# Kernel optimization log

Hardware: AMD Instinct MI355X
Metric: run time of the kernel (lower is better)

## Reference

```python
import jax, jax.numpy as jnp
import numpy as np

B = 65536      # batch
E = 4          # experts per node
F = 32         # per-node input features
H = 256        # hidden width
NODES = 4
D_MID = 128    # intermediate node output dim
D_OUT = 8      # final head dim


def _lin_w(k, fan_in, fan_out):
    b = 1.0 / np.sqrt(fan_in)
    return jax.random.uniform(k, (E, fan_in, fan_out), jnp.float32, -b, b)


def setup_inputs() -> dict:
    key = jax.random.key(0)
    ks = jax.random.split(key, 8)
    feats = jax.random.normal(ks[0], (B, NODES * F), dtype=jnp.float32)
    # routing one-hot blocks embedded in the input vector (as the module expects)
    ohs = [jax.nn.one_hot(jax.random.randint(ks[1 + j], (B,), 0, E), E, dtype=jnp.float32)
           for j in range(NODES)]
    input_val = jnp.concatenate([feats] + ohs, axis=1)  # [B, 144]
    p = {"input_val": input_val}
    kc = iter(jax.random.split(ks[5], 32))
    # node 0: no pre-interface; post: F->H relu, H->D_MID relu
    p["W0_0"] = _lin_w(next(kc), F, H); p["b0_0"] = jnp.full((E, H), 0.1, jnp.float32)
    p["W0_1"] = _lin_w(next(kc), H, D_MID); p["b0_1"] = jnp.full((E, D_MID), 0.1, jnp.float32)
    # nodes 1,2: pre F->H relu; post (D_MID+H)->H relu, H->D_MID relu
    for j in (1, 2):
        p[f"W{j}_pre"] = _lin_w(next(kc), F, H); p[f"b{j}_pre"] = jnp.full((E, H), 0.1, jnp.float32)
        p[f"W{j}_0"] = _lin_w(next(kc), D_MID + H, H); p[f"b{j}_0"] = jnp.full((E, H), 0.1, jnp.float32)
        p[f"W{j}_1"] = _lin_w(next(kc), H, D_MID); p[f"b{j}_1"] = jnp.full((E, D_MID), 0.1, jnp.float32)
    # node 3 (output): pre F->H relu; post (D_MID+H)->H relu, H->D_OUT identity
    p["W3_pre"] = _lin_w(next(kc), F, H); p["b3_pre"] = jnp.full((E, H), 0.1, jnp.float32)
    p["W3_0"] = _lin_w(next(kc), D_MID + H, H); p["b3_0"] = jnp.full((E, H), 0.1, jnp.float32)
    p["W3_1"] = jax.random.uniform(next(kc), (E, H, D_OUT), jnp.float32, -0.003, 0.003)
    p["b3_1"] = jax.random.uniform(next(kc), (E, D_OUT), jnp.float32, -0.003, 0.003)
    return p


def reference(input_val, W0_0, b0_0, W0_1, b0_1,
              W1_pre, b1_pre, W1_0, b1_0, W1_1, b1_1,
              W2_pre, b2_pre, W2_0, b2_0, W2_1, b2_1,
              W3_pre, b3_pre, W3_0, b3_0, W3_1, b3_1):
    relu = jax.nn.relu
    xs = [input_val[:, j * F:(j + 1) * F] for j in range(NODES)]          # per-node features
    ohs = [input_val[:, NODES * F + j * E: NODES * F + (j + 1) * E] for j in range(NODES)]

    def combine(oh, outs):  # oh [B,E] exact one-hot; outs [E,B,D] -> exact per-row expert pick
        return jnp.einsum('be,ebo->bo', oh, outs)

    # node 0 (no previous-level input)
    def n0(W0, b0, W1, b1):
        h = relu(xs[0] @ W0 + b0)
        return relu(h @ W1 + b1)
    x = combine(ohs[0], jax.vmap(n0)(W0_0, b0_0, W0_1, b0_1))  # [B, D_MID]

    def node(xj, xprev, relu_last):
        def f(Wp, bp, W0, b0, W1, b1):
            h = relu(xj @ Wp + bp)                      # pre-interface
            h = jnp.concatenate([xprev, h], axis=-1)    # interface: cat(prev, pre)
            h = relu(h @ W0 + b0)
            o = h @ W1 + b1
            return relu(o) if relu_last else o
        return f

    x = combine(ohs[1], jax.vmap(node(xs[1], x, True))(W1_pre, b1_pre, W1_0, b1_0, W1_1, b1_1))
    x = combine(ohs[2], jax.vmap(node(xs[2], x, True))(W2_pre, b2_pre, W2_0, b2_0, W2_1, b2_1))
    x = combine(ohs[3], jax.vmap(node(xs[3], x, False))(W3_pre, b3_pre, W3_0, b3_0, W3_1, b3_1))
    return x  # [B, D_OUT]
```

## Files before the change

kernel.cpp:

```cpp
#include <hip/hip_runtime.h>
#include <hip/hip_bf16.h>
#include <stdint.h>

typedef unsigned int u32;
typedef unsigned short u16;
typedef unsigned char u8;
typedef __bf16 bf16x8 __attribute__((ext_vector_type(8)));
typedef float f32x4 __attribute__((ext_vector_type(4)));

#define NB 65536
#define NBLK 1280
#define PERM_TOT (NBLK * 64)
#define INVR 0xFFFFFFFFu
#define BLK_DEAD 0xFFFFu

#define O_ROWS 0
#define O_XJ   256
#define O_P    (O_XJ + 4096)
#define O_H    (O_P + 16384)
#define O_RED  O_P
#define SM_BYTES (O_H + 32768)

__device__ __host__ constexpr int TS(int m) {
  constexpr int t[12] = {0, 64, 320, 384, 1152, 1408, 1472, 2240, 2496, 2560, 3328, 3360};
  return t[m];
}

__device__ __forceinline__ u16 f2bf(float f) {
  u32 u = __builtin_bit_cast(u32, f);
  u32 r = (u + 0x7FFFu + ((u >> 16) & 1u)) >> 16;
  return (u16)r;
}
__device__ __forceinline__ float relu_f(float x) { return x > 0.f ? x : 0.f; }
__device__ __forceinline__ f32x4 mfma16(bf16x8 a, bf16x8 b, f32x4 c) {
  return __builtin_amdgcn_mfma_f32_16x16x32_bf16(a, b, c, 0, 0, 0);
}

__device__ __forceinline__ void mkpair(f32x4 acc, float bias, bool dorelu, int l16,
                                       u32& w0, u32& w1) {
  float v0 = acc[0] + bias, v1 = acc[1] + bias, v2 = acc[2] + bias, v3 = acc[3] + bias;
  if (dorelu) { v0 = relu_f(v0); v1 = relu_f(v1); v2 = relu_f(v2); v3 = relu_f(v3); }
  u32 a = (u32)f2bf(v0) | ((u32)f2bf(v1) << 16);
  u32 b = (u32)f2bf(v2) | ((u32)f2bf(v3) << 16);
  u32 ax = (u32)__shfl_xor((int)a, 1);
  u32 bx = (u32)__shfl_xor((int)b, 1);
  if ((l16 & 1) == 0) { w0 = (a & 0xffffu) | (ax << 16); w1 = (a >> 16) | (ax & 0xffff0000u); }
  else                { w0 = (bx & 0xffffu) | (b << 16); w1 = (bx >> 16) | (b & 0xffff0000u); }
}

__device__ __forceinline__ void frag_store_pair(char* base, int KT, int m0, int col,
                                                u32 w0, u32 w1) {
  char* d = base + (((m0 >> 4) * KT + (col >> 5)) << 10) +
            (((m0 & 15) + (((col & 31) >> 3) << 4)) << 4) + (col & 7) * 2;
  *(u32*)d = w0; *(u32*)(d + 16) = w1;
}


struct PrepArgs {
  const float* src[11];
  int K[11], Nsrc[11];
  int tileStart[12];
};

__device__ __forceinline__ void prep_tile_dev(__bf16* __restrict__ pk, const PrepArgs& pa,
                                              int gt, int lane) {
  const int quad = lane >> 4, l16 = lane & 15;
  int m = 0;
  while (gt >= pa.tileStart[m + 1]) m++;
  const int loc = gt - pa.tileStart[m];
  const int K = pa.K[m], Ns = pa.Nsrc[m];
  const int Np = Ns < 16 ? 16 : Ns;
  const int KT = K >> 5, NT = Np >> 4;
  const int e = loc / (KT * NT), rem = loc % (KT * NT);
  const int nt = rem / KT, kt = rem % KT;
  const int k = kt * 32 + quad * 8, n = nt * 16 + l16;
  u32 hw[4];
  if (n < Ns) {
    const float* s = pa.src[m] + ((size_t)e * K + k) * Ns + n;
    u16 h[8];
#pragma unroll
    for (int j = 0; j < 8; j++) h[j] = f2bf(s[(size_t)j * Ns]);
    hw[0] = (u32)h[0] | ((u32)h[1] << 16);
    hw[1] = (u32)h[2] | ((u32)h[3] << 16);
    hw[2] = (u32)h[4] | ((u32)h[5] << 16);
    hw[3] = (u32)h[6] | ((u32)h[7] << 16);
  } else {
    hw[0] = hw[1] = hw[2] = hw[3] = 0u;
  }
  uint4 w; w.x = hw[0]; w.y = hw[1]; w.z = hw[2]; w.w = hw[3];
  *(uint4*)((char*)pk + (size_t)gt * 1024 + lane * 16) = w;
}


__global__ __launch_bounds__(256) void k_front(const float* __restrict__ inp,
                                               u8* __restrict__ bkt,
                                               u32* __restrict__ cnt2,
                                               u32* __restrict__ rank,
                                               __bf16* __restrict__ pk, PrepArgs pa) {
  __shared__ u32 h[256];
  const int tid = threadIdx.x;
  if (blockIdx.x == 0) rank[tid] = 0u;
  h[tid] = 0u;
  __syncthreads();
  const int r = blockIdx.x * 256 + tid;
  const float4* oh = (const float4*)(inp + (size_t)r * 144 + 128);
  u32 b = 0;
#pragma unroll
  for (int j = 0; j < 4; j++) {
    float4 v = oh[j];
    u32 e = v.y > 0.5f ? 1u : (v.z > 0.5f ? 2u : (v.w > 0.5f ? 3u : 0u));
    b |= e << (2 * j);
  }
  bkt[r] = (u8)b;
  atomicAdd(&h[b], 1u);
  __syncthreads();
  cnt2[blockIdx.x * 256 + tid] = h[tid];
  for (int g4 = blockIdx.x; g4 < TS(11) / 4; g4 += 256)
    prep_tile_dev(pk, pa, g4 * 4 + (tid >> 6), tid & 63);
}


__global__ __launch_bounds__(256) void k_place(const u8* __restrict__ bkt,
                                               const u32* __restrict__ cnt2,
                                               u32* __restrict__ rank,
                                               u16* __restrict__ blk2b,
                                               u32* __restrict__ perm) {
  __shared__ u32 s[256], base[256];
  const int tid = threadIdx.x;
  u32 c = 0;
#pragma unroll 8
  for (int j = 0; j < 256; j++) c += cnt2[j * 256 + tid];
  const u32 pad = (c + 63u) & ~63u;
  s[tid] = pad;
  __syncthreads();
  for (int d = 1; d < 256; d <<= 1) {
    u32 v = (tid >= d) ? s[tid - d] : 0u;
    __syncthreads();
    s[tid] += v;
    __syncthreads();
  }
  const u32 off = s[tid] - pad;
  const u32 total = s[255];
  __syncthreads();
  if (blockIdx.x == 0) {
    for (u32 i = off + c; i < off + pad; i++) perm[i] = INVR;
    for (u32 blk = off >> 6; blk < (off + pad) >> 6; blk++) blk2b[blk] = (u16)tid;
    for (u32 blk = (total >> 6) + tid; blk < NBLK; blk += 256) blk2b[blk] = BLK_DEAD;
  }
  s[tid] = 0u;
  __syncthreads();
  const int r = blockIdx.x * 256 + tid;
  const u32 b = bkt[r];
  const u32 lrk = atomicAdd(&s[b], 1u);
  __syncthreads();
  base[tid] = off + (s[tid] ? atomicAdd(&rank[tid], s[tid]) : 0u);
  __syncthreads();
  perm[base[b] + lrk] = (u32)r;
}


__device__ __forceinline__ void xj_load(const float* inp, u32 myrow, int tid, int node,
                                        float4& v0, float4& v1) {
  v0 = make_float4(0.f, 0.f, 0.f, 0.f); v1 = v0;
  if (myrow != INVR) {
    const int c8 = (tid & 3) << 3;
    const float4* p = (const float4*)(inp + (size_t)myrow * 144 + node * 32 + c8);
    v0 = p[0]; v1 = p[1];
  }
}

__device__ __forceinline__ void xj_store(char* sm, int tid, float4 v0, float4 v1) {
  const int r = tid >> 2;
  uint4 w;
  w.x = (u32)f2bf(v0.x) | ((u32)f2bf(v0.y) << 16);
  w.y = (u32)f2bf(v0.z) | ((u32)f2bf(v0.w) << 16);
  w.z = (u32)f2bf(v1.x) | ((u32)f2bf(v1.y) << 16);
  w.w = (u32)f2bf(v1.z) | ((u32)f2bf(v1.w) << 16);
  *(uint4*)(sm + O_XJ + ((r >> 4) << 10) + ((((tid & 3) << 4) + (r & 15)) << 4)) = w;
}

__device__ __forceinline__ void pre_gemm(char* sm, u32 e, int wave, int lane,
                                         const __bf16* Wp, const float* bp) {
  const int l16 = lane & 15;
  const int wn0 = wave * 64;
  const int rsel = ((lane >> 4) << 2) + ((l16 & 1) ? 2 : 0);
  const int colp = l16 & ~1;
  float bias[4];
#pragma unroll
  for (int nt = 0; nt < 4; nt++) bias[nt] = bp[(size_t)e * 256 + wn0 + nt * 16 + l16];
  f32x4 acc[4][4];
#pragma unroll
  for (int i = 0; i < 4; i++)
#pragma unroll
    for (int j = 0; j < 4; j++) acc[i][j] = (f32x4){0.f, 0.f, 0.f, 0.f};
  bf16x8 a[4], b[4];
#pragma unroll
  for (int nt = 0; nt < 4; nt++)
    b[nt] = *(const bf16x8*)(Wp + (size_t)(e * 16 + (wn0 >> 4) + nt) * 512 + lane * 8);
#pragma unroll
  for (int mt = 0; mt < 4; mt++)
    a[mt] = *(const bf16x8*)(sm + O_XJ + (mt << 10) + lane * 16);
#pragma unroll
  for (int mt = 0; mt < 4; mt++)
#pragma unroll
    for (int nt = 0; nt < 4; nt++) acc[mt][nt] = mfma16(a[mt], b[nt], acc[mt][nt]);
#pragma unroll
  for (int nt = 0; nt < 4; nt++) {
    const int n = wn0 + nt * 16;
#pragma unroll
    for (int mt = 0; mt < 4; mt++) {
      u32 w0, w1;
      mkpair(acc[mt][nt], bias[nt], true, l16, w0, w1);
      frag_store_pair(sm + O_H, 8, mt * 16 + rsel, n + colp, w0, w1);
    }
  }
}

__device__ __forceinline__ void main_gemm(char* sm, u32 e, int wave, int lane,
                                          const __bf16* Wm, const float* bm) {
  const int l16 = lane & 15;
  const int wn0 = wave * 64;
  const int rsel = ((lane >> 4) << 2) + ((l16 & 1) ? 2 : 0);
  const int colp = l16 & ~1;
  float bias[4];
#pragma unroll
  for (int nt = 0; nt < 4; nt++) bias[nt] = bm[(size_t)e * 256 + wn0 + nt * 16 + l16];
  f32x4 acc[4][4];
#pragma unroll
  for (int i = 0; i < 4; i++)
#pragma unroll
    for (int j = 0; j < 4; j++) acc[i][j] = (f32x4){0.f, 0.f, 0.f, 0.f};
  const __bf16* bB = Wm + (size_t)(e * 16 + (wn0 >> 4)) * 12 * 512 + lane * 8;
  bf16x8 bb[2][4];
#pragma unroll
  for (int nt = 0; nt < 4; nt++) {
    bb[0][nt] = *(const bf16x8*)(bB + (size_t)(nt * 12 + 0) * 512);
    bb[1][nt] = *(const bf16x8*)(bB + (size_t)(nt * 12 + 1) * 512);
  }
#pragma unroll
  for (int kt = 0; kt < 12; kt++) {
    bf16x8 a[4];
#pragma unroll
    for (int mt = 0; mt < 4; mt++) {
      a[mt] = (kt < 4)
          ? *(const bf16x8*)(sm + O_P + ((mt * 4 + kt) << 10) + lane * 16)
          : *(const bf16x8*)(sm + O_H + ((mt * 8 + (kt - 4)) << 10) + lane * 16);
    }
#pragma unroll
    for (int mt = 0; mt < 4; mt++)
#pragma unroll
      for (int nt = 0; nt < 4; nt++) acc[mt][nt] = mfma16(a[mt], bb[kt & 1][nt], acc[mt][nt]);
    if (kt < 10) {
#pragma unroll
      for (int nt = 0; nt < 4; nt++)
        bb[kt & 1][nt] = *(const bf16x8*)(bB + (size_t)(nt * 12 + kt + 2) * 512);
    }
  }
  __syncthreads();
#pragma unroll
  for (int nt = 0; nt < 4; nt++) {
    const int n = wn0 + nt * 16;
#pragma unroll
    for (int mt = 0; mt < 4; mt++) {
      u32 w0, w1;
      mkpair(acc[mt][nt], bias[nt], true, l16, w0, w1);
      frag_store_pair(sm + O_H, 8, mt * 16 + rsel, n + colp, w0, w1);
    }
  }
  __syncthreads();
}

__device__ __forceinline__ void out_gemm(char* sm, u32 e, int wave, int lane,
                                         const __bf16* Wo, const float* bo) {
  const int l16 = lane & 15;
  const int on0 = wave * 32;
  const int rsel = ((lane >> 4) << 2) + ((l16 & 1) ? 2 : 0);
  const int colp = l16 & ~1;
  float bias[2];
#pragma unroll
  for (int nt = 0; nt < 2; nt++) bias[nt] = bo[(size_t)e * 128 + on0 + nt * 16 + l16];
  f32x4 acc[4][2];
#pragma unroll
  for (int i = 0; i < 4; i++) { acc[i][0] = (f32x4){0.f,0.f,0.f,0.f}; acc[i][1] = acc[i][0]; }
  const __bf16* bB = Wo + (size_t)(e * 8 + (on0 >> 4)) * 8 * 512 + lane * 8;
  bf16x8 bb[2][2];
#pragma unroll
  for (int nt = 0; nt < 2; nt++) {
    bb[0][nt] = *(const bf16x8*)(bB + (size_t)(nt * 8 + 0) * 512);
    bb[1][nt] = *(const bf16x8*)(bB + (size_t)(nt * 8 + 1) * 512);
  }
#pragma unroll
  for (int kt = 0; kt < 8; kt++) {
    bf16x8 a[4];
#pragma unroll
    for (int mt = 0; mt < 4; mt++)
      a[mt] = *(const bf16x8*)(sm + O_H + ((mt * 8 + kt) << 10) + lane * 16);
#pragma unroll
    for (int mt = 0; mt < 4; mt++)
#pragma unroll
      for (int nt = 0; nt < 2; nt++) acc[mt][nt] = mfma16(a[mt], bb[kt & 1][nt], acc[mt][nt]);
    if (kt < 6) {
#pragma unroll
      for (int nt = 0; nt < 2; nt++)
        bb[kt & 1][nt] = *(const bf16x8*)(bB + (size_t)(nt * 8 + kt + 2) * 512);
    }
  }
#pragma unroll
  for (int nt = 0; nt < 2; nt++) {
    const int n = on0 + nt * 16;
#pragma unroll
    for (int mt = 0; mt < 4; mt++) {
      u32 w0, w1;
      mkpair(acc[mt][nt], bias[nt], true, l16, w0, w1);
      frag_store_pair(sm + O_P, 4, mt * 16 + rsel, n + colp, w0, w1);
    }
  }
}

__global__ __launch_bounds__(256, 3) void fused_k(
    const float* __restrict__ inp, const u32* __restrict__ perm,
    const u16* __restrict__ blk2b, const __bf16* __restrict__ pk,
    const float* __restrict__ b0_0, const float* __restrict__ b0_1,
    const float* __restrict__ b1_p, const float* __restrict__ b1_0,
    const float* __restrict__ b1_1, const float* __restrict__ b2_p,
    const float* __restrict__ b2_0, const float* __restrict__ b2_1,
    const float* __restrict__ b3_p, const float* __restrict__ b3_0,
    const float* __restrict__ b3_1, float* __restrict__ dout) {
  const u32 b = blk2b[blockIdx.x];
  if (b == BLK_DEAD) return;
  __shared__ __align__(16) char sm[SM_BYTES];
  u32* rows = (u32*)sm;
  const int tid = threadIdx.x;
  const int wave = tid >> 6, lane = tid & 63, quad = lane >> 4, l16 = lane & 15;
  if (tid < 64) rows[tid] = perm[blockIdx.x * 64 + tid];
  const u32 e0 = b & 3u, e1 = (b >> 2) & 3u, e2 = (b >> 4) & 3u, e3 = (b >> 6) & 3u;
  __syncthreads();
  const u32 myrow = rows[tid >> 2];

  float4 v0, v1;
  xj_load(inp, myrow, tid, 0, v0, v1);
  xj_store(sm, tid, v0, v1);
  __syncthreads();
  pre_gemm(sm, e0, wave, lane, pk + (size_t)TS(0) * 512, b0_0);
  __syncthreads();
  xj_load(inp, myrow, tid, 1, v0, v1);
  out_gemm(sm, e0, wave, lane, pk + (size_t)TS(1) * 512, b0_1);
  xj_store(sm, tid, v0, v1);
  __syncthreads();
  pre_gemm(sm, e1, wave, lane, pk + (size_t)TS(2) * 512, b1_p);
  __syncthreads();
  main_gemm(sm, e1, wave, lane, pk + (size_t)TS(3) * 512, b1_0);
  xj_load(inp, myrow, tid, 2, v0, v1);
  out_gemm(sm, e1, wave, lane, pk + (size_t)TS(4) * 512, b1_1);
  xj_store(sm, tid, v0, v1);
  __syncthreads();
  pre_gemm(sm, e2, wave, lane, pk + (size_t)TS(5) * 512, b2_p);
  __syncthreads();
  main_gemm(sm, e2, wave, lane, pk + (size_t)TS(6) * 512, b2_0);
  xj_load(inp, myrow, tid, 3, v0, v1);
  out_gemm(sm, e2, wave, lane, pk + (size_t)TS(7) * 512, b2_1);
  xj_store(sm, tid, v0, v1);
  __syncthreads();
  pre_gemm(sm, e3, wave, lane, pk + (size_t)TS(8) * 512, b3_p);
  __syncthreads();
  main_gemm(sm, e3, wave, lane, pk + (size_t)TS(9) * 512, b3_0);

  {
    const __bf16* Wo3 = pk + (size_t)TS(10) * 512;
    f32x4 acc3[4];
#pragma unroll
    for (int i = 0; i < 4; i++) acc3[i] = (f32x4){0.f, 0.f, 0.f, 0.f};
#pragma unroll
    for (int kk = 0; kk < 2; kk++) {
      const int kt = wave * 2 + kk;
      bf16x8 b3 = *(const bf16x8*)(Wo3 + (size_t)(e3 * 8 + kt) * 512 + lane * 8);
      bf16x8 a[4];
#pragma unroll
      for (int mt = 0; mt < 4; mt++)
        a[mt] = *(const bf16x8*)(sm + O_H + ((mt * 8 + kt) << 10) + lane * 16);
#pragma unroll
      for (int mt = 0; mt < 4; mt++) acc3[mt] = mfma16(a[mt], b3, acc3[mt]);
    }
#pragma unroll
    for (int mt = 0; mt < 4; mt++)
#pragma unroll
      for (int r = 0; r < 4; r++)
        *(float*)(sm + O_RED +
                  (((size_t)wave * 64 + mt * 16 + quad * 4 + r) * 16 + l16) * 4) = acc3[mt][r];
    __syncthreads();
    const int m = tid >> 2, c = (tid & 3) * 2;
    float s0 = 0.f, s1 = 0.f;
#pragma unroll
    for (int w = 0; w < 4; w++) {
      s0 += *(float*)(sm + O_RED + (((size_t)w * 64 + m) * 16 + c) * 4);
      s1 += *(float*)(sm + O_RED + (((size_t)w * 64 + m) * 16 + c + 1) * 4);
    }
    if (myrow != INVR) {
      float2 o;
      o.x = s0 + b3_1[(size_t)e3 * 8 + c];
      o.y = s1 + b3_1[(size_t)e3 * 8 + c + 1];
      *(float2*)(dout + (size_t)myrow * 8 + c) = o;
    }
  }
}


extern "C" void kernel_launch(void* const* d_in, const int* in_sizes, int n_in,
                              void* d_out, int out_size, void* d_ws, size_t ws_size,
                              hipStream_t stream) {
  (void)in_sizes; (void)n_in; (void)out_size; (void)ws_size;
  const float* inp = (const float*)d_in[0];
  char* ws = (char*)d_ws;

  const size_t oBKT = 0;
  const size_t oRANK = oBKT + NB;
  const size_t oB2B = oRANK + 1024;
  const size_t oCNT2 = (oB2B + NBLK * 2 + 255) & ~(size_t)255;
  const size_t oPERM = oCNT2 + 256 * 256 * 4;
  const size_t oPK = (oPERM + (size_t)PERM_TOT * 4 + 255) & ~(size_t)255;

  u8* bkt = (u8*)(ws + oBKT);
  u32* rank = (u32*)(ws + oRANK);
  u16* blk2b = (u16*)(ws + oB2B);
  u32* cnt2 = (u32*)(ws + oCNT2);
  u32* perm = (u32*)(ws + oPERM);
  __bf16* pk = (__bf16*)(ws + oPK);

  PrepArgs pa;
  const int widx[11] = {1, 3, 5, 7, 9, 11, 13, 15, 17, 19, 21};
  const int Ks[11] = {32, 256, 32, 384, 256, 32, 384, 256, 32, 384, 256};
  const int Ns[11] = {256, 128, 256, 256, 128, 256, 256, 128, 256, 256, 8};
  for (int m = 0; m < 11; m++) {
    pa.src[m] = (const float*)d_in[widx[m]];
    pa.K[m] = Ks[m]; pa.Nsrc[m] = Ns[m]; pa.tileStart[m] = TS(m);
  }
  pa.tileStart[11] = TS(11);

  hipLaunchKernelGGL(k_front, dim3(NB / 256), dim3(256), 0, stream,
                     inp, bkt, cnt2, rank, pk, pa);
  hipLaunchKernelGGL(k_place, dim3(NB / 256), dim3(256), 0, stream,
                     bkt, cnt2, rank, blk2b, perm);
  fused_k<<<NBLK, 256, 0, stream>>>(
      inp, perm, blk2b, pk,
      (const float*)d_in[2], (const float*)d_in[4],
      (const float*)d_in[6], (const float*)d_in[8], (const float*)d_in[10],
      (const float*)d_in[12], (const float*)d_in[14], (const float*)d_in[16],
      (const float*)d_in[18], (const float*)d_in[20], (const float*)d_in[22],
      (float*)d_out);
}
```

Before: 224.6 us.

## Use 512-thread blocks with eight waves splitting GEMM output columns

Doubles the fused kernel's block size to 512 threads so eight waves each compute half as many output columns in the pre, main and output GEMMs. Input staging and the final reduction stay on the first 256 threads or four waves. The aim is more wave-level parallelism and latency hiding per block with fewer accumulator registers per wave. The cost is that each wave now loads the same A fragments from LDS for half the MFMA work, and more threads take part in every barrier.

```diff
diff --git a/kernel.cpp b/kernel.cpp
--- a/kernel.cpp
+++ b/kernel.cpp
@@ -162,7 +162,7 @@
 __device__ __forceinline__ void xj_load(const float* inp, u32 myrow, int tid, int node,
                                         float4& v0, float4& v1) {
   v0 = make_float4(0.f, 0.f, 0.f, 0.f); v1 = v0;
-  if (myrow != INVR) {
+  if (tid < 256 && myrow != INVR) {
     const int c8 = (tid & 3) << 3;
     const float4* p = (const float4*)(inp + (size_t)myrow * 144 + node * 32 + c8);
     v0 = p[0]; v1 = p[1];
@@ -170,6 +170,7 @@
 }
 
 __device__ __forceinline__ void xj_store(char* sm, int tid, float4 v0, float4 v1) {
+  if (tid >= 256) return;
   const int r = tid >> 2;
   uint4 w;
   w.x = (u32)f2bf(v0.x) | ((u32)f2bf(v0.y) << 16);
@@ -182,20 +183,18 @@
 __device__ __forceinline__ void pre_gemm(char* sm, u32 e, int wave, int lane,
                                          const __bf16* Wp, const float* bp) {
   const int l16 = lane & 15;
-  const int wn0 = wave * 64;
+  const int wn0 = wave * 32;
   const int rsel = ((lane >> 4) << 2) + ((l16 & 1) ? 2 : 0);
   const int colp = l16 & ~1;
-  float bias[4];
-#pragma unroll
-  for (int nt = 0; nt < 4; nt++) bias[nt] = bp[(size_t)e * 256 + wn0 + nt * 16 + l16];
-  f32x4 acc[4][4];
-#pragma unroll
-  for (int i = 0; i < 4; i++)
-#pragma unroll
-    for (int j = 0; j < 4; j++) acc[i][j] = (f32x4){0.f, 0.f, 0.f, 0.f};
-  bf16x8 a[4], b[4];
-#pragma unroll
-  for (int nt = 0; nt < 4; nt++)
+  float bias[2];
+#pragma unroll
+  for (int nt = 0; nt < 2; nt++) bias[nt] = bp[(size_t)e * 256 + wn0 + nt * 16 + l16];
+  f32x4 acc[4][2];
+#pragma unroll
+  for (int i = 0; i < 4; i++) { acc[i][0] = (f32x4){0.f,0.f,0.f,0.f}; acc[i][1] = acc[i][0]; }
+  bf16x8 a[4], b[2];
+#pragma unroll
+  for (int nt = 0; nt < 2; nt++)
     b[nt] = *(const bf16x8*)(Wp + (size_t)(e * 16 + (wn0 >> 4) + nt) * 512 + lane * 8);
 #pragma unroll
   for (int mt = 0; mt < 4; mt++)
@@ -203,9 +202,9 @@
 #pragma unroll
   for (int mt = 0; mt < 4; mt++)
 #pragma unroll
-    for (int nt = 0; nt < 4; nt++) acc[mt][nt] = mfma16(a[mt], b[nt], acc[mt][nt]);
-#pragma unroll
-  for (int nt = 0; nt < 4; nt++) {
+    for (int nt = 0; nt < 2; nt++) acc[mt][nt] = mfma16(a[mt], b[nt], acc[mt][nt]);
+#pragma unroll
+  for (int nt = 0; nt < 2; nt++) {
     const int n = wn0 + nt * 16;
 #pragma unroll
     for (int mt = 0; mt < 4; mt++) {
@@ -219,21 +218,19 @@
 __device__ __forceinline__ void main_gemm(char* sm, u32 e, int wave, int lane,
                                           const __bf16* Wm, const float* bm) {
   const int l16 = lane & 15;
-  const int wn0 = wave * 64;
+  const int wn0 = wave * 32;
   const int rsel = ((lane >> 4) << 2) + ((l16 & 1) ? 2 : 0);
   const int colp = l16 & ~1;
-  float bias[4];
-#pragma unroll
-  for (int nt = 0; nt < 4; nt++) bias[nt] = bm[(size_t)e * 256 + wn0 + nt * 16 + l16];
-  f32x4 acc[4][4];
-#pragma unroll
-  for (int i = 0; i < 4; i++)
-#pragma unroll
-    for (int j = 0; j < 4; j++) acc[i][j] = (f32x4){0.f, 0.f, 0.f, 0.f};
+  float bias[2];
+#pragma unroll
+  for (int nt = 0; nt < 2; nt++) bias[nt] = bm[(size_t)e * 256 + wn0 + nt * 16 + l16];
+  f32x4 acc[4][2];
+#pragma unroll
+  for (int i = 0; i < 4; i++) { acc[i][0] = (f32x4){0.f,0.f,0.f,0.f}; acc[i][1] = acc[i][0]; }
   const __bf16* bB = Wm + (size_t)(e * 16 + (wn0 >> 4)) * 12 * 512 + lane * 8;
-  bf16x8 bb[2][4];
-#pragma unroll
-  for (int nt = 0; nt < 4; nt++) {
+  bf16x8 bb[2][2];
+#pragma unroll
+  for (int nt = 0; nt < 2; nt++) {
     bb[0][nt] = *(const bf16x8*)(bB + (size_t)(nt * 12 + 0) * 512);
     bb[1][nt] = *(const bf16x8*)(bB + (size_t)(nt * 12 + 1) * 512);
   }
@@ -249,16 +246,16 @@
 #pragma unroll
     for (int mt = 0; mt < 4; mt++)
 #pragma unroll
-      for (int nt = 0; nt < 4; nt++) acc[mt][nt] = mfma16(a[mt], bb[kt & 1][nt], acc[mt][nt]);
+      for (int nt = 0; nt < 2; nt++) acc[mt][nt] = mfma16(a[mt], bb[kt & 1][nt], acc[mt][nt]);
     if (kt < 10) {
 #pragma unroll
-      for (int nt = 0; nt < 4; nt++)
+      for (int nt = 0; nt < 2; nt++)
         bb[kt & 1][nt] = *(const bf16x8*)(bB + (size_t)(nt * 12 + kt + 2) * 512);
     }
   }
   __syncthreads();
 #pragma unroll
-  for (int nt = 0; nt < 4; nt++) {
+  for (int nt = 0; nt < 2; nt++) {
     const int n = wn0 + nt * 16;
 #pragma unroll
     for (int mt = 0; mt < 4; mt++) {
@@ -273,22 +270,17 @@
 __device__ __forceinline__ void out_gemm(char* sm, u32 e, int wave, int lane,
                                          const __bf16* Wo, const float* bo) {
   const int l16 = lane & 15;
-  const int on0 = wave * 32;
+  const int on0 = wave * 16;
   const int rsel = ((lane >> 4) << 2) + ((l16 & 1) ? 2 : 0);
   const int colp = l16 & ~1;
-  float bias[2];
-#pragma unroll
-  for (int nt = 0; nt < 2; nt++) bias[nt] = bo[(size_t)e * 128 + on0 + nt * 16 + l16];
-  f32x4 acc[4][2];
-#pragma unroll
-  for (int i = 0; i < 4; i++) { acc[i][0] = (f32x4){0.f,0.f,0.f,0.f}; acc[i][1] = acc[i][0]; }
+  const float bias0 = bo[(size_t)e * 128 + on0 + l16];
+  f32x4 acc[4];
+#pragma unroll
+  for (int i = 0; i < 4; i++) acc[i] = (f32x4){0.f, 0.f, 0.f, 0.f};
   const __bf16* bB = Wo + (size_t)(e * 8 + (on0 >> 4)) * 8 * 512 + lane * 8;
-  bf16x8 bb[2][2];
-#pragma unroll
-  for (int nt = 0; nt < 2; nt++) {
-    bb[0][nt] = *(const bf16x8*)(bB + (size_t)(nt * 8 + 0) * 512);
-    bb[1][nt] = *(const bf16x8*)(bB + (size_t)(nt * 8 + 1) * 512);
-  }
+  bf16x8 bb[2];
+  bb[0] = *(const bf16x8*)(bB);
+  bb[1] = *(const bf16x8*)(bB + 512);
 #pragma unroll
   for (int kt = 0; kt < 8; kt++) {
     bf16x8 a[4];
@@ -296,28 +288,18 @@
     for (int mt = 0; mt < 4; mt++)
       a[mt] = *(const bf16x8*)(sm + O_H + ((mt * 8 + kt) << 10) + lane * 16);
 #pragma unroll
-    for (int mt = 0; mt < 4; mt++)
-#pragma unroll
-      for (int nt = 0; nt < 2; nt++) acc[mt][nt] = mfma16(a[mt], bb[kt & 1][nt], acc[mt][nt]);
-    if (kt < 6) {
-#pragma unroll
-      for (int nt = 0; nt < 2; nt++)
-        bb[kt & 1][nt] = *(const bf16x8*)(bB + (size_t)(nt * 8 + kt + 2) * 512);
-    }
-  }
-#pragma unroll
-  for (int nt = 0; nt < 2; nt++) {
-    const int n = on0 + nt * 16;
-#pragma unroll
-    for (int mt = 0; mt < 4; mt++) {
-      u32 w0, w1;
-      mkpair(acc[mt][nt], bias[nt], true, l16, w0, w1);
-      frag_store_pair(sm + O_P, 4, mt * 16 + rsel, n + colp, w0, w1);
-    }
-  }
-}
-
-__global__ __launch_bounds__(256, 3) void fused_k(
+    for (int mt = 0; mt < 4; mt++) acc[mt] = mfma16(a[mt], bb[kt & 1], acc[mt]);
+    if (kt < 6) bb[kt & 1] = *(const bf16x8*)(bB + (size_t)(kt + 2) * 512);
+  }
+#pragma unroll
+  for (int mt = 0; mt < 4; mt++) {
+    u32 w0, w1;
+    mkpair(acc[mt], bias0, true, l16, w0, w1);
+    frag_store_pair(sm + O_P, 4, mt * 16 + rsel, on0 + colp, w0, w1);
+  }
+}
+
+__global__ __launch_bounds__(512, 6) void fused_k(
     const float* __restrict__ inp, const u32* __restrict__ perm,
     const u16* __restrict__ blk2b, const __bf16* __restrict__ pk,
     const float* __restrict__ b0_0, const float* __restrict__ b0_1,
@@ -335,7 +317,7 @@
   if (tid < 64) rows[tid] = perm[blockIdx.x * 64 + tid];
   const u32 e0 = b & 3u, e1 = (b >> 2) & 3u, e2 = (b >> 4) & 3u, e3 = (b >> 6) & 3u;
   __syncthreads();
-  const u32 myrow = rows[tid >> 2];
+  const u32 myrow = rows[(tid & 255) >> 2];
 
   float4 v0, v1;
   xj_load(inp, myrow, tid, 0, v0, v1);
@@ -367,39 +349,43 @@
 
   {
     const __bf16* Wo3 = pk + (size_t)TS(10) * 512;
-    f32x4 acc3[4];
-#pragma unroll
-    for (int i = 0; i < 4; i++) acc3[i] = (f32x4){0.f, 0.f, 0.f, 0.f};
-#pragma unroll
-    for (int kk = 0; kk < 2; kk++) {
-      const int kt = wave * 2 + kk;
-      bf16x8 b3 = *(const bf16x8*)(Wo3 + (size_t)(e3 * 8 + kt) * 512 + lane * 8);
-      bf16x8 a[4];
+    if (wave < 4) {
+      f32x4 acc3[4];
+#pragma unroll
+      for (int i = 0; i < 4; i++) acc3[i] = (f32x4){0.f, 0.f, 0.f, 0.f};
+#pragma unroll
+      for (int kk = 0; kk < 2; kk++) {
+        const int kt = wave * 2 + kk;
+        bf16x8 b3 = *(const bf16x8*)(Wo3 + (size_t)(e3 * 8 + kt) * 512 + lane * 8);
+        bf16x8 a[4];
+#pragma unroll
+        for (int mt = 0; mt < 4; mt++)
+          a[mt] = *(const bf16x8*)(sm + O_H + ((mt * 8 + kt) << 10) + lane * 16);
+#pragma unroll
+        for (int mt = 0; mt < 4; mt++) acc3[mt] = mfma16(a[mt], b3, acc3[mt]);
+      }
 #pragma unroll
       for (int mt = 0; mt < 4; mt++)
-        a[mt] = *(const bf16x8*)(sm + O_H + ((mt * 8 + kt) << 10) + lane * 16);
-#pragma unroll
-      for (int mt = 0; mt < 4; mt++) acc3[mt] = mfma16(a[mt], b3, acc3[mt]);
-    }
-#pragma unroll
-    for (int mt = 0; mt < 4; mt++)
-#pragma unroll
-      for (int r = 0; r < 4; r++)
-        *(float*)(sm + O_RED +
-                  (((size_t)wave * 64 + mt * 16 + quad * 4 + r) * 16 + l16) * 4) = acc3[mt][r];
+#pragma unroll
+        for (int r = 0; r < 4; r++)
+          *(float*)(sm + O_RED +
+                    (((size_t)wave * 64 + mt * 16 + quad * 4 + r) * 16 + l16) * 4) = acc3[mt][r];
+    }
     __syncthreads();
-    const int m = tid >> 2, c = (tid & 3) * 2;
-    float s0 = 0.f, s1 = 0.f;
-#pragma unroll
-    for (int w = 0; w < 4; w++) {
-      s0 += *(float*)(sm + O_RED + (((size_t)w * 64 + m) * 16 + c) * 4);
-      s1 += *(float*)(sm + O_RED + (((size_t)w * 64 + m) * 16 + c + 1) * 4);
-    }
-    if (myrow != INVR) {
-      float2 o;
-      o.x = s0 + b3_1[(size_t)e3 * 8 + c];
-      o.y = s1 + b3_1[(size_t)e3 * 8 + c + 1];
-      *(float2*)(dout + (size_t)myrow * 8 + c) = o;
+    if (tid < 256) {
+      const int m = tid >> 2, c = (tid & 3) * 2;
+      float s0 = 0.f, s1 = 0.f;
+#pragma unroll
+      for (int w = 0; w < 4; w++) {
+        s0 += *(float*)(sm + O_RED + (((size_t)w * 64 + m) * 16 + c) * 4);
+        s1 += *(float*)(sm + O_RED + (((size_t)w * 64 + m) * 16 + c + 1) * 4);
+      }
+      if (myrow != INVR) {
+        float2 o;
+        o.x = s0 + b3_1[(size_t)e3 * 8 + c];
+        o.y = s1 + b3_1[(size_t)e3 * 8 + c + 1];
+        *(float2*)(dout + (size_t)myrow * 8 + c) = o;
+      }
     }
   }
 }
@@ -440,7 +426,7 @@
                      inp, bkt, cnt2, rank, pk, pa);
   hipLaunchKernelGGL(k_place, dim3(NB / 256), dim3(256), 0, stream,
                      bkt, cnt2, rank, blk2b, perm);
-  fused_k<<<NBLK, 256, 0, stream>>>(
+  fused_k<<<NBLK, 512, 0, stream>>>(
       inp, perm, blk2b, pk,
       (const float*)d_in[2], (const float*)d_in[4],
       (const float*)d_in[6], (const float*)d_in[8], (const float*)d_in[10],
```

Measured after the change: 221.5 us. No clear change (-1.3%).

## Halve per-block row tile to 32 rows, raise occupancy, use packed bf16 convert

Applied to the files above, without the earlier changes.

Shrinks each fused block from 64 to 32 routed rows. This doubles the block count, halves shared memory and accumulator registers, and raises the launch-bounds occupancy hint from 3 to 6. Bucket padding becomes 32 rows, which reduces wasted padded rows across the 256 expert-combination buckets. The software-pipelined weight prefetch is dropped in favour of per-iteration loads, and float-to-bf16 conversion uses the v_cvt_pk_bf16_f32 instruction. Trade-off: weights are reloaded per 32 rows, so weight traffic per row doubles, and half the threads sit idle during input staging.

```diff
diff --git a/kernel.cpp b/kernel.cpp
--- a/kernel.cpp
+++ b/kernel.cpp
@@ -9,17 +9,16 @@
 typedef float f32x4 __attribute__((ext_vector_type(4)));
 
 #define NB 65536
-#define NBLK 1280
-#define PERM_TOT (NBLK * 64)
+#define NBLK 2560
+#define PERM_TOT (NBLK * 32)
 #define INVR 0xFFFFFFFFu
 #define BLK_DEAD 0xFFFFu
 
-#define O_ROWS 0
 #define O_XJ   256
-#define O_P    (O_XJ + 4096)
-#define O_H    (O_P + 16384)
+#define O_P    (O_XJ + 2048)
+#define O_H    (O_P + 8192)
 #define O_RED  O_P
-#define SM_BYTES (O_H + 32768)
+#define SM_BYTES (O_H + 16384)
 
 __device__ __host__ constexpr int TS(int m) {
   constexpr int t[12] = {0, 64, 320, 384, 1152, 1408, 1472, 2240, 2496, 2560, 3328, 3360};
@@ -31,17 +30,22 @@
   u32 r = (u + 0x7FFFu + ((u >> 16) & 1u)) >> 16;
   return (u16)r;
 }
+__device__ __forceinline__ u32 cvtpk(float lo, float hi) {
+  u32 r;
+  asm("v_cvt_pk_bf16_f32 %0, %1, %2" : "=v"(r) : "v"(lo), "v"(hi));
+  return r;
+}
 __device__ __forceinline__ float relu_f(float x) { return x > 0.f ? x : 0.f; }
 __device__ __forceinline__ f32x4 mfma16(bf16x8 a, bf16x8 b, f32x4 c) {
   return __builtin_amdgcn_mfma_f32_16x16x32_bf16(a, b, c, 0, 0, 0);
 }
 
-__device__ __forceinline__ void mkpair(f32x4 acc, float bias, bool dorelu, int l16,
+__device__ __forceinline__ void mkpair(f32x4 acc, float bias, int l16,
                                        u32& w0, u32& w1) {
-  float v0 = acc[0] + bias, v1 = acc[1] + bias, v2 = acc[2] + bias, v3 = acc[3] + bias;
-  if (dorelu) { v0 = relu_f(v0); v1 = relu_f(v1); v2 = relu_f(v2); v3 = relu_f(v3); }
-  u32 a = (u32)f2bf(v0) | ((u32)f2bf(v1) << 16);
-  u32 b = (u32)f2bf(v2) | ((u32)f2bf(v3) << 16);
+  float v0 = relu_f(acc[0] + bias), v1 = relu_f(acc[1] + bias);
+  float v2 = relu_f(acc[2] + bias), v3 = relu_f(acc[3] + bias);
+  u32 a = cvtpk(v0, v1);
+  u32 b = cvtpk(v2, v3);
   u32 ax = (u32)__shfl_xor((int)a, 1);
   u32 bx = (u32)__shfl_xor((int)b, 1);
   if ((l16 & 1) == 0) { w0 = (a & 0xffffu) | (ax << 16); w1 = (a >> 16) | (ax & 0xffff0000u); }
@@ -130,7 +134,7 @@
   u32 c = 0;
 #pragma unroll 8
   for (int j = 0; j < 256; j++) c += cnt2[j * 256 + tid];
-  const u32 pad = (c + 63u) & ~63u;
+  const u32 pad = (c + 31u) & ~31u;
   s[tid] = pad;
   __syncthreads();
   for (int d = 1; d < 256; d <<= 1) {
@@ -144,8 +148,8 @@
   __syncthreads();
   if (blockIdx.x == 0) {
     for (u32 i = off + c; i < off + pad; i++) perm[i] = INVR;
-    for (u32 blk = off >> 6; blk < (off + pad) >> 6; blk++) blk2b[blk] = (u16)tid;
-    for (u32 blk = (total >> 6) + tid; blk < NBLK; blk += 256) blk2b[blk] = BLK_DEAD;
+    for (u32 blk = off >> 5; blk < (off + pad) >> 5; blk++) blk2b[blk] = (u16)tid;
+    for (u32 blk = (total >> 5) + tid; blk < NBLK; blk += 256) blk2b[blk] = BLK_DEAD;
   }
   s[tid] = 0u;
   __syncthreads();
@@ -162,7 +166,7 @@
 __device__ __forceinline__ void xj_load(const float* inp, u32 myrow, int tid, int node,
                                         float4& v0, float4& v1) {
   v0 = make_float4(0.f, 0.f, 0.f, 0.f); v1 = v0;
-  if (myrow != INVR) {
+  if (tid < 128 && myrow != INVR) {
     const int c8 = (tid & 3) << 3;
     const float4* p = (const float4*)(inp + (size_t)myrow * 144 + node * 32 + c8);
     v0 = p[0]; v1 = p[1];
@@ -170,12 +174,13 @@
 }
 
 __device__ __forceinline__ void xj_store(char* sm, int tid, float4 v0, float4 v1) {
+  if (tid >= 128) return;
   const int r = tid >> 2;
   uint4 w;
-  w.x = (u32)f2bf(v0.x) | ((u32)f2bf(v0.y) << 16);
-  w.y = (u32)f2bf(v0.z) | ((u32)f2bf(v0.w) << 16);
-  w.z = (u32)f2bf(v1.x) | ((u32)f2bf(v1.y) << 16);
-  w.w = (u32)f2bf(v1.z) | ((u32)f2bf(v1.w) << 16);
+  w.x = cvtpk(v0.x, v0.y);
+  w.y = cvtpk(v0.z, v0.w);
+  w.z = cvtpk(v1.x, v1.y);
+  w.w = cvtpk(v1.z, v1.w);
   *(uint4*)(sm + O_XJ + ((r >> 4) << 10) + ((((tid & 3) << 4) + (r & 15)) << 4)) = w;
 }
 
@@ -188,29 +193,29 @@
   float bias[4];
 #pragma unroll
   for (int nt = 0; nt < 4; nt++) bias[nt] = bp[(size_t)e * 256 + wn0 + nt * 16 + l16];
-  f32x4 acc[4][4];
-#pragma unroll
-  for (int i = 0; i < 4; i++)
+  f32x4 acc[2][4];
+#pragma unroll
+  for (int i = 0; i < 2; i++)
 #pragma unroll
     for (int j = 0; j < 4; j++) acc[i][j] = (f32x4){0.f, 0.f, 0.f, 0.f};
-  bf16x8 a[4], b[4];
+  bf16x8 a[2], b[4];
 #pragma unroll
   for (int nt = 0; nt < 4; nt++)
-    b[nt] = *(const bf16x8*)(Wp + (size_t)(e * 16 + (wn0 >> 4) + nt) * 512 + lane * 8);
-#pragma unroll
-  for (int mt = 0; mt < 4; mt++)
+    b[nt] = *(const bf16x8*)(Wp + (size_t)(e * 16 + wave * 4 + nt) * 512 + lane * 8);
+#pragma unroll
+  for (int mt = 0; mt < 2; mt++)
     a[mt] = *(const bf16x8*)(sm + O_XJ + (mt << 10) + lane * 16);
 #pragma unroll
-  for (int mt = 0; mt < 4; mt++)
+  for (int mt = 0; mt < 2; mt++)
 #pragma unroll
     for (int nt = 0; nt < 4; nt++) acc[mt][nt] = mfma16(a[mt], b[nt], acc[mt][nt]);
 #pragma unroll
   for (int nt = 0; nt < 4; nt++) {
     const int n = wn0 + nt * 16;
 #pragma unroll
-    for (int mt = 0; mt < 4; mt++) {
+    for (int mt = 0; mt < 2; mt++) {
       u32 w0, w1;
-      mkpair(acc[mt][nt], bias[nt], true, l16, w0, w1);
+      mkpair(acc[mt][nt], bias[nt], l16, w0, w1);
       frag_store_pair(sm + O_H, 8, mt * 16 + rsel, n + colp, w0, w1);
     }
   }
@@ -225,45 +230,37 @@
   float bias[4];
 #pragma unroll
   for (int nt = 0; nt < 4; nt++) bias[nt] = bm[(size_t)e * 256 + wn0 + nt * 16 + l16];
-  f32x4 acc[4][4];
-#pragma unroll
-  for (int i = 0; i < 4; i++)
+  f32x4 acc[2][4];
+#pragma unroll
+  for (int i = 0; i < 2; i++)
 #pragma unroll
     for (int j = 0; j < 4; j++) acc[i][j] = (f32x4){0.f, 0.f, 0.f, 0.f};
-  const __bf16* bB = Wm + (size_t)(e * 16 + (wn0 >> 4)) * 12 * 512 + lane * 8;
-  bf16x8 bb[2][4];
-#pragma unroll
-  for (int nt = 0; nt < 4; nt++) {
-    bb[0][nt] = *(const bf16x8*)(bB + (size_t)(nt * 12 + 0) * 512);
-    bb[1][nt] = *(const bf16x8*)(bB + (size_t)(nt * 12 + 1) * 512);
-  }
+  const __bf16* bB = Wm + (size_t)(e * 16 + wave * 4) * 12 * 512 + lane * 8;
 #pragma unroll
   for (int kt = 0; kt < 12; kt++) {
-    bf16x8 a[4];
-#pragma unroll
-    for (int mt = 0; mt < 4; mt++) {
+    bf16x8 a[2], bb[4];
+#pragma unroll
+    for (int mt = 0; mt < 2; mt++) {
       a[mt] = (kt < 4)
           ? *(const bf16x8*)(sm + O_P + ((mt * 4 + kt) << 10) + lane * 16)
           : *(const bf16x8*)(sm + O_H + ((mt * 8 + (kt - 4)) << 10) + lane * 16);
     }
 #pragma unroll
-    for (int mt = 0; mt < 4; mt++)
-#pragma unroll
-      for (int nt = 0; nt < 4; nt++) acc[mt][nt] = mfma16(a[mt], bb[kt & 1][nt], acc[mt][nt]);
-    if (kt < 10) {
-#pragma unroll
-      for (int nt = 0; nt < 4; nt++)
-        bb[kt & 1][nt] = *(const bf16x8*)(bB + (size_t)(nt * 12 + kt + 2) * 512);
-    }
+    for (int nt = 0; nt < 4; nt++)
+      bb[nt] = *(const bf16x8*)(bB + (size_t)(nt * 12 + kt) * 512);
+#pragma unroll
+    for (int mt = 0; mt < 2; mt++)
+#pragma unroll
+      for (int nt = 0; nt < 4; nt++) acc[mt][nt] = mfma16(a[mt], bb[nt], acc[mt][nt]);
   }
   __syncthreads();
 #pragma unroll
   for (int nt = 0; nt < 4; nt++) {
     const int n = wn0 + nt * 16;
 #pragma unroll
-    for (int mt = 0; mt < 4; mt++) {
+    for (int mt = 0; mt < 2; mt++) {
       u32 w0, w1;
-      mkpair(acc[mt][nt], bias[nt], true, l16, w0, w1);
+      mkpair(acc[mt][nt], bias[nt], l16, w0, w1);
       frag_store_pair(sm + O_H, 8, mt * 16 + rsel, n + colp, w0, w1);
     }
   }
@@ -279,45 +276,37 @@
   float bias[2];
 #pragma unroll
   for (int nt = 0; nt < 2; nt++) bias[nt] = bo[(size_t)e * 128 + on0 + nt * 16 + l16];
-  f32x4 acc[4][2];
-#pragma unroll
-  for (int i = 0; i < 4; i++) { acc[i][0] = (f32x4){0.f,0.f,0.f,0.f}; acc[i][1] = acc[i][0]; }
-  const __bf16* bB = Wo + (size_t)(e * 8 + (on0 >> 4)) * 8 * 512 + lane * 8;
-  bf16x8 bb[2][2];
-#pragma unroll
-  for (int nt = 0; nt < 2; nt++) {
-    bb[0][nt] = *(const bf16x8*)(bB + (size_t)(nt * 8 + 0) * 512);
-    bb[1][nt] = *(const bf16x8*)(bB + (size_t)(nt * 8 + 1) * 512);
-  }
+  f32x4 acc[2][2];
+#pragma unroll
+  for (int i = 0; i < 2; i++) { acc[i][0] = (f32x4){0.f,0.f,0.f,0.f}; acc[i][1] = acc[i][0]; }
+  const __bf16* bB = Wo + (size_t)(e * 8 + wave * 2) * 8 * 512 + lane * 8;
 #pragma unroll
   for (int kt = 0; kt < 8; kt++) {
-    bf16x8 a[4];
-#pragma unroll
-    for (int mt = 0; mt < 4; mt++)
+    bf16x8 a[2], bb[2];
+#pragma unroll
+    for (int mt = 0; mt < 2; mt++)
       a[mt] = *(const bf16x8*)(sm + O_H + ((mt * 8 + kt) << 10) + lane * 16);
 #pragma unroll
-    for (int mt = 0; mt < 4; mt++)
-#pragma unroll
-      for (int nt = 0; nt < 2; nt++) acc[mt][nt] = mfma16(a[mt], bb[kt & 1][nt], acc[mt][nt]);
-    if (kt < 6) {
-#pragma unroll
-      for (int nt = 0; nt < 2; nt++)
-        bb[kt & 1][nt] = *(const bf16x8*)(bB + (size_t)(nt * 8 + kt + 2) * 512);
-    }
+    for (int nt = 0; nt < 2; nt++)
+      bb[nt] = *(const bf16x8*)(bB + (size_t)(nt * 8 + kt) * 512);
+#pragma unroll
+    for (int mt = 0; mt < 2; mt++)
+#pragma unroll
+      for (int nt = 0; nt < 2; nt++) acc[mt][nt] = mfma16(a[mt], bb[nt], acc[mt][nt]);
   }
 #pragma unroll
   for (int nt = 0; nt < 2; nt++) {
     const int n = on0 + nt * 16;
 #pragma unroll
-    for (int mt = 0; mt < 4; mt++) {
+    for (int mt = 0; mt < 2; mt++) {
       u32 w0, w1;
-      mkpair(acc[mt][nt], bias[nt], true, l16, w0, w1);
+      mkpair(acc[mt][nt], bias[nt], l16, w0, w1);
       frag_store_pair(sm + O_P, 4, mt * 16 + rsel, n + colp, w0, w1);
     }
   }
 }
 
-__global__ __launch_bounds__(256, 3) void fused_k(
+__global__ __launch_bounds__(256, 6) void fused_k(
     const float* __restrict__ inp, const u32* __restrict__ perm,
     const u16* __restrict__ blk2b, const __bf16* __restrict__ pk,
     const float* __restrict__ b0_0, const float* __restrict__ b0_1,
@@ -332,10 +321,10 @@
   u32* rows = (u32*)sm;
   const int tid = threadIdx.x;
   const int wave = tid >> 6, lane = tid & 63, quad = lane >> 4, l16 = lane & 15;
-  if (tid < 64) rows[tid] = perm[blockIdx.x * 64 + tid];
+  if (tid < 32) rows[tid] = perm[blockIdx.x * 32 + tid];
   const u32 e0 = b & 3u, e1 = (b >> 2) & 3u, e2 = (b >> 4) & 3u, e3 = (b >> 6) & 3u;
   __syncthreads();
-  const u32 myrow = rows[tid >> 2];
+  const u32 myrow = (tid < 128) ? rows[tid >> 2] : INVR;
 
   float4 v0, v1;
   xj_load(inp, myrow, tid, 0, v0, v1);
@@ -367,39 +356,40 @@
 
   {
     const __bf16* Wo3 = pk + (size_t)TS(10) * 512;
-    f32x4 acc3[4];
-#pragma unroll
-    for (int i = 0; i < 4; i++) acc3[i] = (f32x4){0.f, 0.f, 0.f, 0.f};
+    f32x4 acc3[2];
+    acc3[0] = (f32x4){0.f, 0.f, 0.f, 0.f}; acc3[1] = acc3[0];
 #pragma unroll
     for (int kk = 0; kk < 2; kk++) {
       const int kt = wave * 2 + kk;
       bf16x8 b3 = *(const bf16x8*)(Wo3 + (size_t)(e3 * 8 + kt) * 512 + lane * 8);
-      bf16x8 a[4];
-#pragma unroll
-      for (int mt = 0; mt < 4; mt++)
+      bf16x8 a[2];
+#pragma unroll
+      for (int mt = 0; mt < 2; mt++)
         a[mt] = *(const bf16x8*)(sm + O_H + ((mt * 8 + kt) << 10) + lane * 16);
 #pragma unroll
-      for (int mt = 0; mt < 4; mt++) acc3[mt] = mfma16(a[mt], b3, acc3[mt]);
-    }
-#pragma unroll
-    for (int mt = 0; mt < 4; mt++)
+      for (int mt = 0; mt < 2; mt++) acc3[mt] = mfma16(a[mt], b3, acc3[mt]);
+    }
+#pragma unroll
+    for (int mt = 0; mt < 2; mt++)
 #pragma unroll
       for (int r = 0; r < 4; r++)
         *(float*)(sm + O_RED +
-                  (((size_t)wave * 64 + mt * 16 + quad * 4 + r) * 16 + l16) * 4) = acc3[mt][r];
+                  (((size_t)wave * 32 + mt * 16 + quad * 4 + r) * 16 + l16) * 4) = acc3[mt][r];
     __syncthreads();
-    const int m = tid >> 2, c = (tid & 3) * 2;
-    float s0 = 0.f, s1 = 0.f;
-#pragma unroll
-    for (int w = 0; w < 4; w++) {
-      s0 += *(float*)(sm + O_RED + (((size_t)w * 64 + m) * 16 + c) * 4);
-      s1 += *(float*)(sm + O_RED + (((size_t)w * 64 + m) * 16 + c + 1) * 4);
-    }
-    if (myrow != INVR) {
-      float2 o;
-      o.x = s0 + b3_1[(size_t)e3 * 8 + c];
-      o.y = s1 + b3_1[(size_t)e3 * 8 + c + 1];
-      *(float2*)(dout + (size_t)myrow * 8 + c) = o;
+    if (tid < 128) {
+      const int m = tid >> 2, c = (tid & 3) * 2;
+      float s0 = 0.f, s1 = 0.f;
+#pragma unroll
+      for (int w = 0; w < 4; w++) {
+        s0 += *(float*)(sm + O_RED + (((size_t)w * 32 + m) * 16 + c) * 4);
+        s1 += *(float*)(sm + O_RED + (((size_t)w * 32 + m) * 16 + c + 1) * 4);
+      }
+      if (myrow != INVR) {
+        float2 o;
+        o.x = s0 + b3_1[(size_t)e3 * 8 + c];
+        o.y = s1 + b3_1[(size_t)e3 * 8 + c + 1];
+        *(float2*)(dout + (size_t)myrow * 8 + c) = o;
+      }
     }
   }
 }
```

Measured after the change: 258.5 us. 1.15x slower.
